# Performance work log

Measured on AMD Instinct MI355X. Metric: run time of the kernel, lower is better.

## Reference

```python
import jax, jax.numpy as jnp
import numpy as np

B, N, C, H, D, Kd, Ff, L = 4, 4096, 512, 8, 64, 256, 2048, 2
EPS = 1e-5


def _ln(x, g, b):
    m = x.mean(-1, keepdims=True)
    v = ((x - m) ** 2).mean(-1, keepdims=True)
    return (x - m) / jnp.sqrt(v + EPS) * g + b


def setup_inputs() -> dict:
    key = jax.random.key(0)
    ks = jax.random.split(key, 20)
    s = 0.02
    return {
        'x': jax.random.normal(ks[0], (B, N, C), jnp.float32),
        'Wq': jax.random.normal(ks[1], (L, H, D, C), jnp.float32) * s,
        'Wk': jax.random.normal(ks[2], (L, H, D, C), jnp.float32) * s,
        'Wv': jax.random.normal(ks[3], (L, H, D, C), jnp.float32) * s,
        'Wo': jax.random.normal(ks[4], (L, C, H * D), jnp.float32) * s,
        'bo': jnp.zeros((L, C), jnp.float32),
        'ln1_g': jnp.ones((L, C), jnp.float32),
        'ln1_b': jnp.zeros((L, C), jnp.float32),
        'W1': jax.random.normal(ks[5], (L, Ff, C), jnp.float32) * s,
        'b1': jnp.zeros((L, Ff), jnp.float32),
        'W2': jax.random.normal(ks[6], (L, C, Ff), jnp.float32) * s,
        'b2': jnp.zeros((L, C), jnp.float32),
        'ln2_g': jnp.ones((L, C), jnp.float32),
        'ln2_b': jnp.zeros((L, C), jnp.float32),
        'Ew': jax.random.normal(ks[7], (Kd, N), jnp.float32) * (1.0 / np.sqrt(N)),
        'Eb': jnp.zeros((Kd,), jnp.float32),
    }


def reference(x, Wq, Wk, Wv, Wo, bo, ln1_g, ln1_b, W1, b1, W2, b2, ln2_g, ln2_b, Ew, Eb):
    # Linformer, layerwise-shared E=F projection, causal=False, eval mode (dropout off).
    n_layers = Wq.shape[0]
    d = Wq.shape[2]
    scale = 1.0 / jnp.sqrt(jnp.asarray(d, x.dtype))
    for l in range(n_layers):
        # per-head projections, all heads at once: [b,h,n,d]
        Q = jnp.einsum('bnc,hdc->bhnd', x, Wq[l])
        K = jnp.einsum('bnc,hdc->bhnd', x, Wk[l])
        V = jnp.einsum('bnc,hdc->bhnd', x, Wv[l])
        # E projection along seq axis: K^T [b,h,d,n] -> [b,h,d,k]
        Kp = jnp.einsum('bhnd,kn->bhdk', K, Ew) + Eb[None, None, None, :]
        P = jax.nn.softmax(jnp.einsum('bhnd,bhdk->bhnk', Q, Kp) * scale, axis=-1)
        # F projection (= E, layerwise sharing): V^T -> [b,h,k,d]
        Vp = jnp.einsum('bhnd,kn->bhkd', V, Ew) + Eb[None, None, :, None]
        o = jnp.einsum('bhnk,bhkd->bhnd', P, Vp)
        b_, h_, n_, d_ = o.shape
        o = o.transpose(0, 2, 1, 3).reshape(b_, n_, h_ * d_)  # concat heads
        o = o @ Wo[l].T + bo[l]
        x = _ln(x + o, ln1_g[l], ln1_b[l])  # post-norm residual
        f = jax.nn.gelu(x @ W1[l].T + b1[l], approximate=False) @ W2[l].T + b2[l]
        x = _ln(x + f, ln2_g[l], ln2_b[l])
    return x
```

## Files before the change

kernel.cpp:

```cpp
#include <hip/hip_runtime.h>
#include <math.h>

typedef unsigned short u16;
typedef __attribute__((ext_vector_type(8))) short short8;
typedef __attribute__((ext_vector_type(4))) float f32x4;

#define B_ 4
#define N_ 4096
#define C_ 512
#define H_ 8
#define D_ 64
#define KD_ 256
#define FF_ 2048
#define L_ 2

__device__ __forceinline__ float bf2f(u16 x) {
  return __builtin_bit_cast(float, (unsigned int)x << 16);
}
__device__ __forceinline__ u16 f2bf(float f) {
  unsigned int t = __builtin_bit_cast(unsigned int, f);
  return (u16)((t + 0x7fffu + ((t >> 16) & 1u)) >> 16);
}

#define GLD(g, l)                                                             \
  __builtin_amdgcn_global_load_lds(                                           \
      (const __attribute__((address_space(1))) void*)(g),                     \
      (__attribute__((address_space(3))) void*)(l), 16, 0, 0)

__global__ __launch_bounds__(256) void cvt_kernel(const float* __restrict__ in,
                                                  u16* __restrict__ out, int n4) {
  int i = blockIdx.x * 256 + threadIdx.x;
  if (i >= n4) return;
  float4 v = reinterpret_cast<const float4*>(in)[i];
  ushort4 o;
  o.x = f2bf(v.x); o.y = f2bf(v.y); o.z = f2bf(v.z); o.w = f2bf(v.w);
  reinterpret_cast<ushort4*>(out)[i] = o;
}

__global__ __launch_bounds__(256) void transpose_kernel(const u16* __restrict__ in,
                                                        u16* __restrict__ out) {
  __shared__ u16 T[64][72];
  int n0 = blockIdx.x * 64, c0 = blockIdx.y * 64, b = blockIdx.z;
  const u16* src = in + (long)b * N_ * C_;
  u16* dst = out + (long)b * C_ * N_;
  int t = threadIdx.x;
  int r = t >> 3, cq = (t & 7) * 8;
#pragma unroll
  for (int h = 0; h < 2; ++h) {
    const u16* p = src + (long)(n0 + r + h * 32) * C_ + c0 + cq;
    ushort4 v0 = *reinterpret_cast<const ushort4*>(p);
    ushort4 v1 = *reinterpret_cast<const ushort4*>(p + 4);
    T[r + h * 32][cq + 0] = v0.x; T[r + h * 32][cq + 1] = v0.y;
    T[r + h * 32][cq + 2] = v0.z; T[r + h * 32][cq + 3] = v0.w;
    T[r + h * 32][cq + 4] = v1.x; T[r + h * 32][cq + 5] = v1.y;
    T[r + h * 32][cq + 6] = v1.z; T[r + h * 32][cq + 7] = v1.w;
  }
  __syncthreads();
  int cc = t >> 3, nq = (t & 7) * 8;
#pragma unroll
  for (int h = 0; h < 2; ++h) {
    int cl = cc + h * 32;
    ushort4 w0, w1;
    w0.x = T[nq + 0][cl]; w0.y = T[nq + 1][cl];
    w0.z = T[nq + 2][cl]; w0.w = T[nq + 3][cl];
    w1.x = T[nq + 4][cl]; w1.y = T[nq + 5][cl];
    w1.z = T[nq + 6][cl]; w1.w = T[nq + 7][cl];
    u16* q = dst + (long)(c0 + cl) * N_ + n0 + nq;
    *reinterpret_cast<ushort4*>(q) = w0;
    *reinterpret_cast<ushort4*>(q + 4) = w1;
  }
}

template <int BM, int BN, int EPI, int SPLITK>
__global__ __launch_bounds__(256, 2) void gemm_nt(
    const u16* __restrict__ A, const u16* __restrict__ B, void* __restrict__ Cout,
    const float* __restrict__ bias, int K, int lda, int ldb, int ldc,
    long sA0, long sA1, long sB0, long sB1, long sC0, long sC1, long sCh,
    int nz, float alpha) {
  constexpr int BK = 64;
  constexpr int WM = BM / 2, WN = BN / 2;
  constexpr int FM = WM / 16, FN = WN / 16;
  constexpr int CA = BM / 32, CB = BN / 32;

  __shared__ __attribute__((aligned(16))) u16 As[BM * BK];
  __shared__ __attribute__((aligned(16))) u16 Bs[BN * BK];

  int z, chunk;
  if constexpr (SPLITK > 1) { z = blockIdx.z % nz; chunk = blockIdx.z / nz; }
  else { z = blockIdx.z; chunk = 0; }
  int zb = z >> 3, zh = z & 7;
  A += (long)zb * sA0 + (long)zh * sA1;
  B += (long)zb * sB0 + (long)zh * sB1;
  long coff = (long)zb * sC0 + (long)zh * sC1 + (long)chunk * sCh;

  int tid = threadIdx.x;
  int lane = tid & 63, wid = tid >> 6;
  int wr = wid >> 1, wc = wid & 1;
  int row0 = blockIdx.x * BM, col0 = blockIdx.y * BN;

  int Kc = K / SPLITK;
  int kbeg = chunk * Kc;

  f32x4 acc[FM][FN] = {};

  for (int k0 = kbeg; k0 < kbeg + Kc; k0 += BK) {
#pragma unroll
    for (int i = 0; i < CA; ++i) {
      int c = tid + i * 256;
      GLD(A + (long)(row0 + (c >> 3)) * lda + k0 + (c & 7) * 8, As + c * 8);
    }
#pragma unroll
    for (int i = 0; i < CB; ++i) {
      int c = tid + i * 256;
      GLD(B + (long)(col0 + (c >> 3)) * ldb + k0 + (c & 7) * 8, Bs + c * 8);
    }
    __syncthreads();

    int lr = lane & 15, lk = (lane >> 4) * 8;
#pragma unroll
    for (int kk = 0; kk < BK; kk += 32) {
      short8 af[FM], bfr[FN];
#pragma unroll
      for (int mi = 0; mi < FM; ++mi)
        af[mi] = *reinterpret_cast<const short8*>(&As[(wr * WM + mi * 16 + lr) * BK + kk + lk]);
#pragma unroll
      for (int nj = 0; nj < FN; ++nj)
        bfr[nj] = *reinterpret_cast<const short8*>(&Bs[(wc * WN + nj * 16 + lr) * BK + kk + lk]);
#pragma unroll
      for (int mi = 0; mi < FM; ++mi)
#pragma unroll
        for (int nj = 0; nj < FN; ++nj)
          acc[mi][nj] = __builtin_amdgcn_mfma_f32_16x16x32_bf16(af[mi], bfr[nj], acc[mi][nj], 0, 0, 0);
    }
    __syncthreads();
  }

  int lc = lane & 15, rb = (lane >> 4) * 4;
#pragma unroll
  for (int mi = 0; mi < FM; ++mi) {
#pragma unroll
    for (int nj = 0; nj < FN; ++nj) {
      int j = col0 + wc * WN + nj * 16 + lc;
      int m0 = row0 + wr * WM + mi * 16 + rb;
#pragma unroll
      for (int r = 0; r < 4; ++r) {
        int m = m0 + r;
        float v = acc[mi][nj][r];
        if constexpr (EPI == 2) {
          float t = v + bias[j];
          float gl = 0.5f * t * (1.f + erff(t * 0.70710678118f));
          reinterpret_cast<u16*>(Cout)[coff + (long)m * ldc + j] = f2bf(gl);
        } else if constexpr (EPI == 3) {
          float bi = bias ? bias[j] : 0.f;
          reinterpret_cast<u16*>(Cout)[coff + (long)m * ldc + j] = f2bf(v + bi);
        } else if constexpr (EPI == 4) {
          reinterpret_cast<u16*>(Cout)[coff + (long)m * ldc + j] = f2bf(v + bias[m]);
        } else if constexpr (EPI == 6) {
          reinterpret_cast<u16*>(Cout)[coff + (long)j * ldc + m] = f2bf(v + bias[m]);
        } else {
          reinterpret_cast<float*>(Cout)[coff + (long)m * ldc + j] = v;
        }
      }
    }
  }
}

__global__ __launch_bounds__(256) void reduce8_kernel(const float* __restrict__ part,
                                                      u16* __restrict__ out) {
  int i = blockIdx.x * 256 + threadIdx.x;
  const float4* p = reinterpret_cast<const float4*>(part);
  float4 s = p[i];
#pragma unroll
  for (int c = 1; c < 8; ++c) {
    float4 t = p[i + c * 131072];
    s.x += t.x; s.y += t.y; s.z += t.z; s.w += t.w;
  }
  ushort4 o;
  o.x = f2bf(s.x); o.y = f2bf(s.y); o.z = f2bf(s.z); o.w = f2bf(s.w);
  reinterpret_cast<ushort4*>(out)[i] = o;
}

__global__ __launch_bounds__(512, 2) void attn_kernel(
    const u16* __restrict__ Q, const u16* __restrict__ Kp,
    const u16* __restrict__ Vpt, u16* __restrict__ O) {
  constexpr int LQ = 72, LKP = 72, LVP = 264, LP = 264;
  __shared__ __attribute__((aligned(16))) u16 Q_s[128 * LQ];
  __shared__ __attribute__((aligned(16))) u16 Kp_s[256 * LKP];
  __shared__ __attribute__((aligned(16))) u16 Vp_s[64 * LVP];
  __shared__ __attribute__((aligned(16))) u16 P_s[128 * LP];

  int n0 = blockIdx.x * 128;
  int bh = blockIdx.y;
  int b = bh >> 3, h = bh & 7;
  long qbase = ((long)b * N_ + n0) * 512 + h * 64;
  const u16* Kpb = Kp + ((long)b * KD_) * 512 + h * 64;
  const u16* Vpb = Vpt + ((long)b * 512 + h * 64) * KD_;

  int tid = threadIdx.x;
#pragma unroll
  for (int i = 0; i < 2; ++i) {
    int c = tid + i * 512;
    int r = c >> 3, c8 = (c & 7) * 8;
    *reinterpret_cast<uint4*>(&Q_s[r * LQ + c8]) =
        *reinterpret_cast<const uint4*>(Q + qbase + (long)r * 512 + c8);
  }
#pragma unroll
  for (int i = 0; i < 4; ++i) {
    int c = tid + i * 512;
    int r = c >> 3, c8 = (c & 7) * 8;
    *reinterpret_cast<uint4*>(&Kp_s[r * LKP + c8]) =
        *reinterpret_cast<const uint4*>(Kpb + (long)r * 512 + c8);
  }
#pragma unroll
  for (int i = 0; i < 4; ++i) {
    int c = tid + i * 512;
    int r = c >> 5, c8 = (c & 31) * 8;
    *reinterpret_cast<uint4*>(&Vp_s[r * LVP + c8]) =
        *reinterpret_cast<const uint4*>(Vpb + (long)r * KD_ + c8);
  }
  __syncthreads();

  int lane = tid & 63, w = tid >> 6;
  int q0 = w * 16;
  int lr = lane & 15, lk = (lane >> 4) * 8;
  int lc = lane & 15, rb = (lane >> 4) * 4;

  f32x4 acc[16] = {};
  short8 af0 = *reinterpret_cast<const short8*>(&Q_s[(q0 + lr) * LQ + lk]);
  short8 af1 = *reinterpret_cast<const short8*>(&Q_s[(q0 + lr) * LQ + 32 + lk]);
#pragma unroll
  for (int t = 0; t < 16; ++t) {
    short8 b0 = *reinterpret_cast<const short8*>(&Kp_s[(t * 16 + lr) * LKP + lk]);
    short8 b1 = *reinterpret_cast<const short8*>(&Kp_s[(t * 16 + lr) * LKP + 32 + lk]);
    acc[t] = __builtin_amdgcn_mfma_f32_16x16x32_bf16(af0, b0, acc[t], 0, 0, 0);
    acc[t] = __builtin_amdgcn_mfma_f32_16x16x32_bf16(af1, b1, acc[t], 0, 0, 0);
  }

  float mx[4] = {-3.4e38f, -3.4e38f, -3.4e38f, -3.4e38f};
#pragma unroll
  for (int t = 0; t < 16; ++t)
#pragma unroll
    for (int r = 0; r < 4; ++r) {
      acc[t][r] *= 0.125f;
      mx[r] = fmaxf(mx[r], acc[t][r]);
    }
#pragma unroll
  for (int o = 1; o < 16; o <<= 1)
#pragma unroll
    for (int r = 0; r < 4; ++r) mx[r] = fmaxf(mx[r], __shfl_xor(mx[r], o));
  float sm[4] = {0.f, 0.f, 0.f, 0.f};
#pragma unroll
  for (int t = 0; t < 16; ++t)
#pragma unroll
    for (int r = 0; r < 4; ++r) {
      float e = __expf(acc[t][r] - mx[r]);
      acc[t][r] = e;
      sm[r] += e;
    }
#pragma unroll
  for (int o = 1; o < 16; o <<= 1)
#pragma unroll
    for (int r = 0; r < 4; ++r) sm[r] += __shfl_xor(sm[r], o);
  float inv[4];
#pragma unroll
  for (int r = 0; r < 4; ++r) inv[r] = 1.f / sm[r];
#pragma unroll
  for (int t = 0; t < 16; ++t)
#pragma unroll
    for (int r = 0; r < 4; ++r)
      P_s[(q0 + rb + r) * LP + t * 16 + lc] = f2bf(acc[t][r] * inv[r]);

  f32x4 o2[4] = {};
#pragma unroll
  for (int kk = 0; kk < 8; ++kk) {
    short8 pa = *reinterpret_cast<const short8*>(&P_s[(q0 + lr) * LP + kk * 32 + lk]);
#pragma unroll
    for (int nj = 0; nj < 4; ++nj) {
      short8 vb = *reinterpret_cast<const short8*>(&Vp_s[(nj * 16 + lr) * LVP + kk * 32 + lk]);
      o2[nj] = __builtin_amdgcn_mfma_f32_16x16x32_bf16(pa, vb, o2[nj], 0, 0, 0);
    }
  }
#pragma unroll
  for (int nj = 0; nj < 4; ++nj)
#pragma unroll
    for (int r = 0; r < 4; ++r)
      O[qbase + (long)(q0 + rb + r) * 512 + nj * 16 + lc] = f2bf(o2[nj][r]);
}

__global__ __launch_bounds__(256) void add_ln_kernel(
    const float* __restrict__ xin32, const u16* __restrict__ xinb,
    const u16* __restrict__ yin, const float* __restrict__ g,
    const float* __restrict__ bt, float* __restrict__ xout32,
    u16* __restrict__ xbout) {
  int row = blockIdx.x * 4 + (threadIdx.x >> 6);
  int lane = threadIdx.x & 63;
  long base = (long)row * C_ + lane * 8;
  float s[8];
  if (xin32) {
    float4 a0 = *reinterpret_cast<const float4*>(xin32 + base);
    float4 a1 = *reinterpret_cast<const float4*>(xin32 + base + 4);
    s[0] = a0.x; s[1] = a0.y; s[2] = a0.z; s[3] = a0.w;
    s[4] = a1.x; s[5] = a1.y; s[6] = a1.z; s[7] = a1.w;
  } else {
    ushort4 x0 = *reinterpret_cast<const ushort4*>(xinb + base);
    ushort4 x1 = *reinterpret_cast<const ushort4*>(xinb + base + 4);
    s[0] = bf2f(x0.x); s[1] = bf2f(x0.y); s[2] = bf2f(x0.z); s[3] = bf2f(x0.w);
    s[4] = bf2f(x1.x); s[5] = bf2f(x1.y); s[6] = bf2f(x1.z); s[7] = bf2f(x1.w);
  }
  ushort4 u0 = *reinterpret_cast<const ushort4*>(yin + base);
  ushort4 u1 = *reinterpret_cast<const ushort4*>(yin + base + 4);
  s[0] += bf2f(u0.x); s[1] += bf2f(u0.y); s[2] += bf2f(u0.z); s[3] += bf2f(u0.w);
  s[4] += bf2f(u1.x); s[5] += bf2f(u1.y); s[6] += bf2f(u1.z); s[7] += bf2f(u1.w);
  float sum = 0.f;
#pragma unroll
  for (int i = 0; i < 8; ++i) sum += s[i];
#pragma unroll
  for (int o = 1; o < 64; o <<= 1) sum += __shfl_xor(sum, o);
  float mean = sum * (1.f / C_);
  float var = 0.f;
#pragma unroll
  for (int i = 0; i < 8; ++i) { float d = s[i] - mean; var += d * d; }
#pragma unroll
  for (int o = 1; o < 64; o <<= 1) var += __shfl_xor(var, o);
  float inv = rsqrtf(var * (1.f / C_) + 1e-5f);
  int c0 = lane * 8;
  float o[8];
#pragma unroll
  for (int i = 0; i < 8; ++i) o[i] = (s[i] - mean) * inv * g[c0 + i] + bt[c0 + i];
  if (xout32) {
    float4 f0 = {o[0], o[1], o[2], o[3]};
    float4 f1 = {o[4], o[5], o[6], o[7]};
    *reinterpret_cast<float4*>(xout32 + base) = f0;
    *reinterpret_cast<float4*>(xout32 + base + 4) = f1;
  }
  if (xbout) {
    ushort4 w0 = {f2bf(o[0]), f2bf(o[1]), f2bf(o[2]), f2bf(o[3])};
    ushort4 w1 = {f2bf(o[4]), f2bf(o[5]), f2bf(o[6]), f2bf(o[7])};
    *reinterpret_cast<ushort4*>(xbout + base) = w0;
    *reinterpret_cast<ushort4*>(xbout + base + 4) = w1;
  }
}

extern "C" void kernel_launch(void* const* d_in, const int* in_sizes, int n_in,
                              void* d_out, int out_size, void* d_ws, size_t ws_size,
                              hipStream_t stream) {
  const float* x    = (const float*)d_in[0];
  const float* Wq   = (const float*)d_in[1];
  const float* Wk   = (const float*)d_in[2];
  const float* Wv   = (const float*)d_in[3];
  const float* Wo   = (const float*)d_in[4];
  const float* bo   = (const float*)d_in[5];
  const float* ln1g = (const float*)d_in[6];
  const float* ln1b = (const float*)d_in[7];
  const float* W1   = (const float*)d_in[8];
  const float* b1   = (const float*)d_in[9];
  const float* W2   = (const float*)d_in[10];
  const float* b2   = (const float*)d_in[11];
  const float* ln2g = (const float*)d_in[12];
  const float* ln2b = (const float*)d_in[13];
  const float* Ew   = (const float*)d_in[14];
  const float* Eb   = (const float*)d_in[15];
  float* xc = (float*)d_out;

  char* wsp = (char*)d_ws;
  size_t off = 0;
  auto alloc = [&](size_t bytes) -> void* {
    void* p = wsp + off;
    off = (off + bytes + 255) & ~(size_t)255;
    return p;
  };
  u16* xb  = (u16*)alloc(8388608UL * 2);
  u16* BIG = (u16*)alloc(16777216UL * 2);
  u16* Qb  = (u16*)alloc(8388608UL * 2);
  u16* yb  = (u16*)alloc(8388608UL * 2);
  u16* xEb = (u16*)alloc(524288UL * 2);
  u16* Kpb = (u16*)alloc(524288UL * 2);
  u16* Vpt = (u16*)alloc(524288UL * 2);
  u16* wqb = (u16*)alloc(524288UL * 2);
  u16* wkb = (u16*)alloc(524288UL * 2);
  u16* wvb = (u16*)alloc(524288UL * 2);
  u16* wob = (u16*)alloc(524288UL * 2);
  u16* w1b = (u16*)alloc(2097152UL * 2);
  u16* w2b = (u16*)alloc(2097152UL * 2);
  u16* ewb = (u16*)alloc(1048576UL * 2);
  (void)ws_size; (void)in_sizes; (void)n_in; (void)out_size;

  auto cvt = [&](const float* src, u16* dst, long n) {
    int n4 = (int)(n / 4);
    cvt_kernel<<<dim3((n4 + 255) / 256), dim3(256), 0, stream>>>(src, dst, n4);
  };
  cvt(x, xb, 8388608);
  cvt(Wq, wqb, 524288);
  cvt(Wk, wkb, 524288);
  cvt(Wv, wvb, 524288);
  cvt(Wo, wob, 524288);
  cvt(W1, w1b, 2097152);
  cvt(W2, w2b, 2097152);
  cvt(Ew, ewb, 1048576);

  for (int l = 0; l < L_; ++l) {
    const u16* wq = wqb + (long)l * 262144;
    const u16* wk = wkb + (long)l * 262144;
    const u16* wv = wvb + (long)l * 262144;
    const u16* wo = wob + (long)l * 262144;
    const u16* w1 = w1b + (long)l * 1048576;
    const u16* w2 = w2b + (long)l * 1048576;

    u16* xT = BIG;
    float* partF = (float*)(BIG + 8388608);
    transpose_kernel<<<dim3(64, 8, 4), dim3(256), 0, stream>>>(xb, xT);
    gemm_nt<128, 128, 7, 8><<<dim3(2, 4, 32), dim3(256), 0, stream>>>(
        ewb, xT, partF, nullptr, 4096, 4096, 4096, 512,
        0, 0, 0, 2097152, 0, 131072, 524288, 4, 1.f);
    reduce8_kernel<<<dim3(512), dim3(256), 0, stream>>>(partF, xEb);
    gemm_nt<128, 128, 4, 1><<<dim3(2, 4, 4), dim3(256), 0, stream>>>(
        xEb, wk, Kpb, Eb, 512, 512, 512, 512,
        0, 131072, 0, 0, 0, 131072, 0, 4, 1.f);
    gemm_nt<128, 128, 6, 1><<<dim3(2, 4, 4), dim3(256), 0, stream>>>(
        xEb, wv, Vpt, Eb, 512, 512, 512, 256,
        0, 131072, 0, 0, 0, 131072, 0, 4, 1.f);
    gemm_nt<128, 128, 3, 1><<<dim3(128, 4, 1), dim3(256), 0, stream>>>(
        xb, wq, Qb, nullptr, 512, 512, 512, 512,
        0, 0, 0, 0, 0, 0, 0, 1, 1.f);

    attn_kernel<<<dim3(32, 32), dim3(512), 0, stream>>>(Qb, Kpb, Vpt, Qb);

    gemm_nt<128, 128, 3, 1><<<dim3(128, 4, 1), dim3(256), 0, stream>>>(
        Qb, wo, yb, bo + (long)l * 512, 512, 512, 512, 512,
        0, 0, 0, 0, 0, 0, 0, 1, 1.f);
    add_ln_kernel<<<dim3(4096), dim3(256), 0, stream>>>(
        l == 0 ? x : nullptr, l == 0 ? nullptr : xb, yb,
        ln1g + (long)l * 512, ln1b + (long)l * 512, nullptr, xb);

    for (int ch = 0; ch < 2; ++ch) {
      u16* h1 = BIG;
      const u16* xch = xb + (long)ch * 4194304;
      gemm_nt<128, 128, 2, 1><<<dim3(64, 16, 1), dim3(256), 0, stream>>>(
          xch, w1, h1, b1 + (long)l * 2048, 512, 512, 512, 2048,
          0, 0, 0, 0, 0, 0, 0, 1, 1.f);
      gemm_nt<128, 64, 3, 1><<<dim3(64, 8, 1), dim3(256), 0, stream>>>(
          h1, w2, yb + (long)ch * 4194304, b2 + (long)l * 512,
          2048, 2048, 2048, 512, 0, 0, 0, 0, 0, 0, 0, 1, 1.f);
    }
    add_ln_kernel<<<dim3(4096), dim3(256), 0, stream>>>(
        nullptr, xb, yb, ln2g + (long)l * 512, ln2b + (long)l * 512,
        (l == L_ - 1) ? xc : nullptr, (l == L_ - 1) ? (u16*)nullptr : xb);
  }
}
```

Before: 635.3 us.

## Add 256x256 double-buffered ping-pong GEMM for Q, O and FFN1 projections

Introduces a 512-thread GEMM kernel with 256x256 tiles, double-buffered LDS fed by direct global-to-LDS loads, interleaved prefetch between MFMA phases with barriers and wave priority, and an XCD-aware block swizzle. It replaces the 128x128 GEMM for the Q, output and first FFN projections to raise data reuse and overlap loads with compute. The FFN1 GELU epilogue switches from erf to a tanh approximation, cheaper but slightly different numerically. Small-N GEMMs launch only 128 workgroups, which may underfill the device.

```diff
diff --git a/kernel.cpp b/kernel.cpp
--- a/kernel.cpp
+++ b/kernel.cpp
@@ -26,6 +26,8 @@
   __builtin_amdgcn_global_load_lds(                                           \
       (const __attribute__((address_space(1))) void*)(g),                     \
       (__attribute__((address_space(3))) void*)(l), 16, 0, 0)
+
+#define MFMA16 __builtin_amdgcn_mfma_f32_16x16x32_bf16
 
 __global__ __launch_bounds__(256) void cvt_kernel(const float* __restrict__ in,
                                                   u16* __restrict__ out, int n4) {
@@ -71,6 +73,145 @@
   }
 }
 
+template <int EPI>
+__global__ __launch_bounds__(512, 2) void gemm256_nt(
+    const u16* __restrict__ A, const u16* __restrict__ B, u16* __restrict__ C,
+    const float* __restrict__ bias, int K, int lda, int ldb, int ldc) {
+  __shared__ __attribute__((aligned(16))) u16 As[2 * 16384];
+  __shared__ __attribute__((aligned(16))) u16 Bs[2 * 16384];
+
+  int gy = gridDim.y;
+  int nwg = gridDim.x * gy;
+  int id = blockIdx.x * gy + blockIdx.y;
+  int q = nwg >> 3;
+  int nid = (id & 7) * q + (id >> 3);
+  int row0 = (nid / gy) * 256, col0 = (nid % gy) * 256;
+
+  int tid = threadIdx.x;
+  int lane = tid & 63, wid = tid >> 6;
+  int wr = wid >> 2, wc = wid & 3;
+  int lr = lane & 15, lk = (lane >> 4) * 8;
+
+  int ar0 = tid >> 3, ac0 = (tid & 7) * 8;
+  int f1 = tid + 512;
+  int ar1 = f1 >> 3, ac1 = (f1 & 7) * 8;
+
+  auto stageA = [&](int d, int h, int k0) {
+    GLD(A + (long)(row0 + h * 128 + ar0) * lda + k0 + ac0,
+        As + d * 16384 + h * 8192 + tid * 8);
+    GLD(A + (long)(row0 + h * 128 + ar1) * lda + k0 + ac1,
+        As + d * 16384 + h * 8192 + f1 * 8);
+  };
+  auto stageB = [&](int d, int h, int k0) {
+    GLD(B + (long)(col0 + h * 128 + ar0) * ldb + k0 + ac0,
+        Bs + d * 16384 + h * 8192 + tid * 8);
+    GLD(B + (long)(col0 + h * 128 + ar1) * ldb + k0 + ac1,
+        Bs + d * 16384 + h * 8192 + f1 * 8);
+  };
+
+  f32x4 acc[8][4] = {};
+  int NT = K >> 6;
+
+  stageA(0, 0, 0); stageA(0, 1, 0); stageB(0, 0, 0); stageB(0, 1, 0);
+
+  for (int t = 0; t < NT; ++t) {
+    int cur = t & 1, nxt = cur ^ 1;
+    const u16* Ab = As + cur * 16384;
+    const u16* Bb = Bs + cur * 16384;
+    int k1 = (t + 1) << 6;
+    bool pf = (t + 1 < NT);
+
+    asm volatile("s_waitcnt vmcnt(0)" ::: "memory");
+    __builtin_amdgcn_s_barrier();
+
+    short8 bf0[4], bf1[4], af[4];
+#pragma unroll
+    for (int nj = 0; nj < 4; ++nj)
+      bf0[nj] = *reinterpret_cast<const short8*>(&Bb[(wc * 64 + nj * 16 + lr) * 64 + lk]);
+#pragma unroll
+    for (int mi = 0; mi < 4; ++mi)
+      af[mi] = *reinterpret_cast<const short8*>(&Ab[(wr * 128 + mi * 16 + lr) * 64 + lk]);
+    if (pf) stageA(nxt, 0, k1);
+    __builtin_amdgcn_s_barrier();
+    __builtin_amdgcn_s_setprio(1);
+#pragma unroll
+    for (int mi = 0; mi < 4; ++mi)
+#pragma unroll
+      for (int nj = 0; nj < 4; ++nj)
+        acc[mi][nj] = MFMA16(af[mi], bf0[nj], acc[mi][nj], 0, 0, 0);
+    __builtin_amdgcn_s_setprio(0);
+    __builtin_amdgcn_s_barrier();
+#pragma unroll
+    for (int mi = 0; mi < 4; ++mi)
+      af[mi] = *reinterpret_cast<const short8*>(&Ab[(wr * 128 + (mi + 4) * 16 + lr) * 64 + lk]);
+    if (pf) stageA(nxt, 1, k1);
+    __builtin_amdgcn_s_barrier();
+    __builtin_amdgcn_s_setprio(1);
+#pragma unroll
+    for (int mi = 0; mi < 4; ++mi)
+#pragma unroll
+      for (int nj = 0; nj < 4; ++nj)
+        acc[mi + 4][nj] = MFMA16(af[mi], bf0[nj], acc[mi + 4][nj], 0, 0, 0);
+    __builtin_amdgcn_s_setprio(0);
+    __builtin_amdgcn_s_barrier();
+#pragma unroll
+    for (int nj = 0; nj < 4; ++nj)
+      bf1[nj] = *reinterpret_cast<const short8*>(&Bb[(wc * 64 + nj * 16 + lr) * 64 + 32 + lk]);
+#pragma unroll
+    for (int mi = 0; mi < 4; ++mi)
+      af[mi] = *reinterpret_cast<const short8*>(&Ab[(wr * 128 + mi * 16 + lr) * 64 + 32 + lk]);
+    if (pf) stageB(nxt, 0, k1);
+    __builtin_amdgcn_s_barrier();
+    __builtin_amdgcn_s_setprio(1);
+#pragma unroll
+    for (int mi = 0; mi < 4; ++mi)
+#pragma unroll
+      for (int nj = 0; nj < 4; ++nj)
+        acc[mi][nj] = MFMA16(af[mi], bf1[nj], acc[mi][nj], 0, 0, 0);
+    __builtin_amdgcn_s_setprio(0);
+    __builtin_amdgcn_s_barrier();
+#pragma unroll
+    for (int mi = 0; mi < 4; ++mi)
+      af[mi] = *reinterpret_cast<const short8*>(&Ab[(wr * 128 + (mi + 4) * 16 + lr) * 64 + 32 + lk]);
+    if (pf) stageB(nxt, 1, k1);
+    __builtin_amdgcn_s_barrier();
+    __builtin_amdgcn_s_setprio(1);
+#pragma unroll
+    for (int mi = 0; mi < 4; ++mi)
+#pragma unroll
+      for (int nj = 0; nj < 4; ++nj)
+        acc[mi + 4][nj] = MFMA16(af[mi], bf1[nj], acc[mi + 4][nj], 0, 0, 0);
+    __builtin_amdgcn_s_setprio(0);
+    __builtin_amdgcn_s_barrier();
+  }
+
+  int lc = lane & 15, rb = (lane >> 4) * 4;
+#pragma unroll
+  for (int mi = 0; mi < 8; ++mi) {
+#pragma unroll
+    for (int nj = 0; nj < 4; ++nj) {
+      int j = col0 + wc * 64 + nj * 16 + lc;
+      int m0 = row0 + wr * 128 + mi * 16 + rb;
+#pragma unroll
+      for (int r = 0; r < 4; ++r) {
+        int m = m0 + r;
+        float v = acc[mi][nj][r];
+        if constexpr (EPI == 0) {
+          C[(long)m * ldc + j] = f2bf(v);
+        } else if constexpr (EPI == 1) {
+          C[(long)m * ldc + j] = f2bf(v + bias[j]);
+        } else {
+          float tt = v + bias[j];
+          float u = tt * (0.7978845608f + 0.0356774081f * tt * tt);
+          float e = __expf(2.f * u);
+          float th = 1.f - 2.f / (e + 1.f);
+          C[(long)m * ldc + j] = f2bf(0.5f * tt * (1.f + th));
+        }
+      }
+    }
+  }
+}
+
 template <int BM, int BN, int EPI, int SPLITK>
 __global__ __launch_bounds__(256, 2) void gemm_nt(
     const u16* __restrict__ A, const u16* __restrict__ B, void* __restrict__ Cout,
@@ -130,7 +271,7 @@
       for (int mi = 0; mi < FM; ++mi)
 #pragma unroll
         for (int nj = 0; nj < FN; ++nj)
-          acc[mi][nj] = __builtin_amdgcn_mfma_f32_16x16x32_bf16(af[mi], bfr[nj], acc[mi][nj], 0, 0, 0);
+          acc[mi][nj] = MFMA16(af[mi], bfr[nj], acc[mi][nj], 0, 0, 0);
     }
     __syncthreads();
   }
@@ -146,11 +287,7 @@
       for (int r = 0; r < 4; ++r) {
         int m = m0 + r;
         float v = acc[mi][nj][r];
-        if constexpr (EPI == 2) {
-          float t = v + bias[j];
-          float gl = 0.5f * t * (1.f + erff(t * 0.70710678118f));
-          reinterpret_cast<u16*>(Cout)[coff + (long)m * ldc + j] = f2bf(gl);
-        } else if constexpr (EPI == 3) {
+        if constexpr (EPI == 3) {
           float bi = bias ? bias[j] : 0.f;
           reinterpret_cast<u16*>(Cout)[coff + (long)m * ldc + j] = f2bf(v + bi);
         } else if constexpr (EPI == 4) {
@@ -232,8 +369,8 @@
   for (int t = 0; t < 16; ++t) {
     short8 b0 = *reinterpret_cast<const short8*>(&Kp_s[(t * 16 + lr) * LKP + lk]);
     short8 b1 = *reinterpret_cast<const short8*>(&Kp_s[(t * 16 + lr) * LKP + 32 + lk]);
-    acc[t] = __builtin_amdgcn_mfma_f32_16x16x32_bf16(af0, b0, acc[t], 0, 0, 0);
-    acc[t] = __builtin_amdgcn_mfma_f32_16x16x32_bf16(af1, b1, acc[t], 0, 0, 0);
+    acc[t] = MFMA16(af0, b0, acc[t], 0, 0, 0);
+    acc[t] = MFMA16(af1, b1, acc[t], 0, 0, 0);
   }
 
   float mx[4] = {-3.4e38f, -3.4e38f, -3.4e38f, -3.4e38f};
@@ -277,7 +414,7 @@
 #pragma unroll
     for (int nj = 0; nj < 4; ++nj) {
       short8 vb = *reinterpret_cast<const short8*>(&Vp_s[(nj * 16 + lr) * LVP + kk * 32 + lk]);
-      o2[nj] = __builtin_amdgcn_mfma_f32_16x16x32_bf16(pa, vb, o2[nj], 0, 0, 0);
+      o2[nj] = MFMA16(pa, vb, o2[nj], 0, 0, 0);
     }
   }
 #pragma unroll
@@ -419,15 +556,13 @@
     gemm_nt<128, 128, 6, 1><<<dim3(2, 4, 4), dim3(256), 0, stream>>>(
         xEb, wv, Vpt, Eb, 512, 512, 512, 256,
         0, 131072, 0, 0, 0, 131072, 0, 4, 1.f);
-    gemm_nt<128, 128, 3, 1><<<dim3(128, 4, 1), dim3(256), 0, stream>>>(
-        xb, wq, Qb, nullptr, 512, 512, 512, 512,
-        0, 0, 0, 0, 0, 0, 0, 1, 1.f);
+    gemm256_nt<0><<<dim3(64, 2), dim3(512), 0, stream>>>(
+        xb, wq, Qb, nullptr, 512, 512, 512, 512);
 
     attn_kernel<<<dim3(32, 32), dim3(512), 0, stream>>>(Qb, Kpb, Vpt, Qb);
 
-    gemm_nt<128, 128, 3, 1><<<dim3(128, 4, 1), dim3(256), 0, stream>>>(
-        Qb, wo, yb, bo + (long)l * 512, 512, 512, 512, 512,
-        0, 0, 0, 0, 0, 0, 0, 1, 1.f);
+    gemm256_nt<1><<<dim3(64, 2), dim3(512), 0, stream>>>(
+        Qb, wo, yb, bo + (long)l * 512, 512, 512, 512, 512);
     add_ln_kernel<<<dim3(4096), dim3(256), 0, stream>>>(
         l == 0 ? x : nullptr, l == 0 ? nullptr : xb, yb,
         ln1g + (long)l * 512, ln1b + (long)l * 512, nullptr, xb);
@@ -435,9 +570,8 @@
     for (int ch = 0; ch < 2; ++ch) {
       u16* h1 = BIG;
       const u16* xch = xb + (long)ch * 4194304;
-      gemm_nt<128, 128, 2, 1><<<dim3(64, 16, 1), dim3(256), 0, stream>>>(
-          xch, w1, h1, b1 + (long)l * 2048, 512, 512, 512, 2048,
-          0, 0, 0, 0, 0, 0, 0, 1, 1.f);
+      gemm256_nt<2><<<dim3(32, 8), dim3(512), 0, stream>>>(
+          xch, w1, h1, b1 + (long)l * 2048, 512, 512, 512, 2048);
       gemm_nt<128, 64, 3, 1><<<dim3(64, 8, 1), dim3(256), 0, stream>>>(
           h1, w2, yb + (long)ch * 4194304, b2 + (long)l * 512,
           2048, 2048, 2048, 512, 0, 0, 0, 0, 0, 0, 0, 1, 1.f);
```

New measurement: 626.5 us. Within noise of the previous version (-1.4%).

## Add 4-stage pipelined 256-row GEMM and split FFN along hidden dim

Applied to the files above, without the earlier changes.

Adds a new 512-thread GEMM kernel with a 4-deep global-to-LDS ring buffer, XOR-swizzled LDS layout, explicit vmcnt waits and barriers, setprio around the MFMA blocks, and a workgroup-id remap for L2 locality. The Q, output-projection and FFN GEMMs move to it. The FFN is now split along the hidden dimension rather than rows, with the first half's W2 partial kept in fp32 scratch and added in the second half's epilogue. The GELU epilogue switches from erf to a tanh approximation with __expf, which is cheaper but departs slightly from the exact reference.

```diff
diff --git a/kernel.cpp b/kernel.cpp
--- a/kernel.cpp
+++ b/kernel.cpp
@@ -26,6 +26,8 @@
   __builtin_amdgcn_global_load_lds(                                           \
       (const __attribute__((address_space(1))) void*)(g),                     \
       (__attribute__((address_space(3))) void*)(l), 16, 0, 0)
+
+#define MFMA16 __builtin_amdgcn_mfma_f32_16x16x32_bf16
 
 __global__ __launch_bounds__(256) void cvt_kernel(const float* __restrict__ in,
                                                   u16* __restrict__ out, int n4) {
@@ -71,6 +73,136 @@
   }
 }
 
+template <int BN, int WM, int WN, int EPI>
+__global__ __launch_bounds__(512, 2) void gemm8p(
+    const u16* __restrict__ A, const u16* __restrict__ B, u16* __restrict__ C,
+    const float* __restrict__ bias, const float* __restrict__ acc32,
+    float* __restrict__ out32, int K, int lda, int ldb, int ldc) {
+  constexpr int BM = 256, BK = 32;
+  constexpr int GB = (BN * BK) / (512 * 8);
+  constexpr int G = 2 + GB;
+  constexpr int FM = WM / 16, FN = WN / 16;
+  constexpr int NWN = BN / WN;
+  constexpr int FM0 = FM / 2;
+
+  __shared__ __attribute__((aligned(16))) u16 As[4][BM * BK];
+  __shared__ __attribute__((aligned(16))) u16 Bs[4][BN * BK];
+
+  int gy = gridDim.y;
+  int nwg = gridDim.x * gy;
+  int id = blockIdx.x * gy + blockIdx.y;
+  int nid = (id & 7) * (nwg >> 3) + (id >> 3);
+  int row0 = (nid / gy) * BM, col0 = (nid % gy) * BN;
+
+  int tid = threadIdx.x;
+  int lane = tid & 63, wid = tid >> 6;
+  int wr = wid / NWN, wc = wid % NWN;
+  int lr = lane & 15, q = lane >> 4;
+
+  auto stA = [&](int buf, int k0) {
+#pragma unroll
+    for (int g = 0; g < 2; ++g) {
+      int c = g * 512 + tid;
+      int r = c >> 2, ck = c & 3;
+      GLD(A + (long)(row0 + r) * lda + k0 + ((ck ^ ((r >> 1) & 3)) << 3),
+          &As[buf][c * 8]);
+    }
+  };
+  auto stB = [&](int buf, int k0) {
+#pragma unroll
+    for (int g = 0; g < GB; ++g) {
+      int c = g * 512 + tid;
+      int r = c >> 2, ck = c & 3;
+      GLD(B + (long)(col0 + r) * ldb + k0 + ((ck ^ ((r >> 1) & 3)) << 3),
+          &Bs[buf][c * 8]);
+    }
+  };
+  auto rd = [&](const u16* Tb, int r) {
+    return *reinterpret_cast<const short8*>(&Tb[r * 32 + ((q ^ ((r >> 1) & 3)) << 3)]);
+  };
+
+  f32x4 acc[FM][FN] = {};
+  int NT = K / BK;
+
+  stA(0, 0); stB(0, 0);
+  stA(1, BK); stB(1, BK);
+  stA(2, 2 * BK); stB(2, 2 * BK);
+
+  for (int t = 0; t < NT; ++t) {
+    const u16* Ab = As[t & 3];
+    const u16* Bb = Bs[t & 3];
+    bool pf = (t + 3) < NT;
+    int bn = (t + 3) & 3, kn = (t + 3) * BK;
+
+    if constexpr (G == 4) asm volatile("s_waitcnt vmcnt(8)" ::: "memory");
+    else                  asm volatile("s_waitcnt vmcnt(6)" ::: "memory");
+    __builtin_amdgcn_s_barrier();
+
+    short8 bf[FN], af[FM0];
+#pragma unroll
+    for (int nj = 0; nj < FN; ++nj) bf[nj] = rd(Bb, wc * WN + nj * 16 + lr);
+#pragma unroll
+    for (int mi = 0; mi < FM0; ++mi) af[mi] = rd(Ab, wr * WM + mi * 16 + lr);
+    if (pf) stA(bn, kn);
+    __builtin_amdgcn_s_barrier();
+    asm volatile("s_waitcnt lgkmcnt(0)" ::: "memory");
+    __builtin_amdgcn_sched_barrier(0);
+    __builtin_amdgcn_s_setprio(1);
+#pragma unroll
+    for (int mi = 0; mi < FM0; ++mi)
+#pragma unroll
+      for (int nj = 0; nj < FN; ++nj)
+        acc[mi][nj] = MFMA16(af[mi], bf[nj], acc[mi][nj], 0, 0, 0);
+    __builtin_amdgcn_s_setprio(0);
+    __builtin_amdgcn_s_barrier();
+#pragma unroll
+    for (int mi = 0; mi < FM - FM0; ++mi)
+      af[mi] = rd(Ab, wr * WM + (FM0 + mi) * 16 + lr);
+    if (pf) stB(bn, kn);
+    __builtin_amdgcn_s_barrier();
+    asm volatile("s_waitcnt lgkmcnt(0)" ::: "memory");
+    __builtin_amdgcn_sched_barrier(0);
+    __builtin_amdgcn_s_setprio(1);
+#pragma unroll
+    for (int mi = 0; mi < FM - FM0; ++mi)
+#pragma unroll
+      for (int nj = 0; nj < FN; ++nj)
+        acc[FM0 + mi][nj] = MFMA16(af[mi], bf[nj], acc[FM0 + mi][nj], 0, 0, 0);
+    __builtin_amdgcn_s_setprio(0);
+    __builtin_amdgcn_s_barrier();
+  }
+
+  int lc = lane & 15, rb = (lane >> 4) * 4;
+#pragma unroll
+  for (int mi = 0; mi < FM; ++mi) {
+#pragma unroll
+    for (int nj = 0; nj < FN; ++nj) {
+      int j = col0 + wc * WN + nj * 16 + lc;
+      int m0 = row0 + wr * WM + mi * 16 + rb;
+#pragma unroll
+      for (int r = 0; r < 4; ++r) {
+        long m = m0 + r;
+        float v = acc[mi][nj][r];
+        if constexpr (EPI == 0) {
+          C[m * ldc + j] = f2bf(v);
+        } else if constexpr (EPI == 1) {
+          C[m * ldc + j] = f2bf(v + bias[j]);
+        } else if constexpr (EPI == 2) {
+          float tt = v + bias[j];
+          float u = tt * (0.7978845608f + 0.0356774081f * tt * tt);
+          float e = __expf(2.f * u);
+          float th = 1.f - 2.f / (e + 1.f);
+          C[m * ldc + j] = f2bf(0.5f * tt * (1.f + th));
+        } else if constexpr (EPI == 8) {
+          out32[m * ldc + j] = v;
+        } else {
+          C[m * ldc + j] = f2bf(v + acc32[m * ldc + j] + bias[j]);
+        }
+      }
+    }
+  }
+}
+
 template <int BM, int BN, int EPI, int SPLITK>
 __global__ __launch_bounds__(256, 2) void gemm_nt(
     const u16* __restrict__ A, const u16* __restrict__ B, void* __restrict__ Cout,
@@ -130,7 +262,7 @@
       for (int mi = 0; mi < FM; ++mi)
 #pragma unroll
         for (int nj = 0; nj < FN; ++nj)
-          acc[mi][nj] = __builtin_amdgcn_mfma_f32_16x16x32_bf16(af[mi], bfr[nj], acc[mi][nj], 0, 0, 0);
+          acc[mi][nj] = MFMA16(af[mi], bfr[nj], acc[mi][nj], 0, 0, 0);
     }
     __syncthreads();
   }
@@ -146,14 +278,7 @@
       for (int r = 0; r < 4; ++r) {
         int m = m0 + r;
         float v = acc[mi][nj][r];
-        if constexpr (EPI == 2) {
-          float t = v + bias[j];
-          float gl = 0.5f * t * (1.f + erff(t * 0.70710678118f));
-          reinterpret_cast<u16*>(Cout)[coff + (long)m * ldc + j] = f2bf(gl);
-        } else if constexpr (EPI == 3) {
-          float bi = bias ? bias[j] : 0.f;
-          reinterpret_cast<u16*>(Cout)[coff + (long)m * ldc + j] = f2bf(v + bi);
-        } else if constexpr (EPI == 4) {
+        if constexpr (EPI == 4) {
           reinterpret_cast<u16*>(Cout)[coff + (long)m * ldc + j] = f2bf(v + bias[m]);
         } else if constexpr (EPI == 6) {
           reinterpret_cast<u16*>(Cout)[coff + (long)j * ldc + m] = f2bf(v + bias[m]);
@@ -232,8 +357,8 @@
   for (int t = 0; t < 16; ++t) {
     short8 b0 = *reinterpret_cast<const short8*>(&Kp_s[(t * 16 + lr) * LKP + lk]);
     short8 b1 = *reinterpret_cast<const short8*>(&Kp_s[(t * 16 + lr) * LKP + 32 + lk]);
-    acc[t] = __builtin_amdgcn_mfma_f32_16x16x32_bf16(af0, b0, acc[t], 0, 0, 0);
-    acc[t] = __builtin_amdgcn_mfma_f32_16x16x32_bf16(af1, b1, acc[t], 0, 0, 0);
+    acc[t] = MFMA16(af0, b0, acc[t], 0, 0, 0);
+    acc[t] = MFMA16(af1, b1, acc[t], 0, 0, 0);
   }
 
   float mx[4] = {-3.4e38f, -3.4e38f, -3.4e38f, -3.4e38f};
@@ -277,7 +402,7 @@
 #pragma unroll
     for (int nj = 0; nj < 4; ++nj) {
       short8 vb = *reinterpret_cast<const short8*>(&Vp_s[(nj * 16 + lr) * LVP + kk * 32 + lk]);
-      o2[nj] = __builtin_amdgcn_mfma_f32_16x16x32_bf16(pa, vb, o2[nj], 0, 0, 0);
+      o2[nj] = MFMA16(pa, vb, o2[nj], 0, 0, 0);
     }
   }
 #pragma unroll
@@ -419,28 +544,29 @@
     gemm_nt<128, 128, 6, 1><<<dim3(2, 4, 4), dim3(256), 0, stream>>>(
         xEb, wv, Vpt, Eb, 512, 512, 512, 256,
         0, 131072, 0, 0, 0, 131072, 0, 4, 1.f);
-    gemm_nt<128, 128, 3, 1><<<dim3(128, 4, 1), dim3(256), 0, stream>>>(
-        xb, wq, Qb, nullptr, 512, 512, 512, 512,
-        0, 0, 0, 0, 0, 0, 0, 1, 1.f);
+    gemm8p<128, 64, 64, 0><<<dim3(64, 4), dim3(512), 0, stream>>>(
+        xb, wq, Qb, nullptr, nullptr, nullptr, 512, 512, 512, 512);
 
     attn_kernel<<<dim3(32, 32), dim3(512), 0, stream>>>(Qb, Kpb, Vpt, Qb);
 
-    gemm_nt<128, 128, 3, 1><<<dim3(128, 4, 1), dim3(256), 0, stream>>>(
-        Qb, wo, yb, bo + (long)l * 512, 512, 512, 512, 512,
-        0, 0, 0, 0, 0, 0, 0, 1, 1.f);
+    gemm8p<128, 64, 64, 1><<<dim3(64, 4), dim3(512), 0, stream>>>(
+        Qb, wo, yb, bo + (long)l * 512, nullptr, nullptr, 512, 512, 512, 512);
     add_ln_kernel<<<dim3(4096), dim3(256), 0, stream>>>(
         l == 0 ? x : nullptr, l == 0 ? nullptr : xb, yb,
         ln1g + (long)l * 512, ln1b + (long)l * 512, nullptr, xb);
 
     for (int ch = 0; ch < 2; ++ch) {
       u16* h1 = BIG;
-      const u16* xch = xb + (long)ch * 4194304;
-      gemm_nt<128, 128, 2, 1><<<dim3(64, 16, 1), dim3(256), 0, stream>>>(
-          xch, w1, h1, b1 + (long)l * 2048, 512, 512, 512, 2048,
-          0, 0, 0, 0, 0, 0, 0, 1, 1.f);
-      gemm_nt<128, 64, 3, 1><<<dim3(64, 8, 1), dim3(256), 0, stream>>>(
-          h1, w2, yb + (long)ch * 4194304, b2 + (long)l * 512,
-          2048, 2048, 2048, 512, 0, 0, 0, 0, 0, 0, 0, 1, 1.f);
+      gemm8p<256, 128, 64, 2><<<dim3(64, 4), dim3(512), 0, stream>>>(
+          xb, w1 + (long)ch * 1024 * 512, h1, b1 + (long)l * 2048 + ch * 1024,
+          nullptr, nullptr, 512, 512, 512, 1024);
+      if (ch == 0) {
+        gemm8p<128, 64, 64, 8><<<dim3(64, 4), dim3(512), 0, stream>>>(
+            h1, w2 + 0, nullptr, nullptr, nullptr, xc, 1024, 1024, 2048, 512);
+      } else {
+        gemm8p<128, 64, 64, 9><<<dim3(64, 4), dim3(512), 0, stream>>>(
+            h1, w2 + 1024, yb, b2 + (long)l * 512, xc, nullptr, 1024, 1024, 2048, 512);
+      }
     }
     add_ln_kernel<<<dim3(4096), dim3(256), 0, stream>>>(
         nullptr, xb, yb, ln2g + (long)l * 512, ln2b + (long)l * 512,
```

After: 588.2 us. -7.4%, faster.
